# Kernel optimization log

Hardware: AMD Instinct MI355X
Metric: run time of the kernel (lower is better)

## Reference

```python
import jax, jax.numpy as jnp
import numpy as np

B, FEAT, FIELD, K = 16384, 2048, 32, 64

def setup_inputs() -> dict:
    key = jax.random.key(0)
    k1, k2, k3, k4 = jax.random.split(key, 4)
    x = jax.random.normal(k1, (B, FEAT), dtype=jnp.float32)
    # nn.Linear(feature_size, 1): weight [1, FEAT] (use vector), bias [1] (scalar)
    w = jax.random.normal(k2, (FEAT,), dtype=jnp.float32) / np.sqrt(FEAT)
    b = jax.random.normal(k3, (), dtype=jnp.float32)
    # v ~ N(0, 0.01) as in torch.normal(0, 0.01, ...)
    v = 0.01 * jax.random.normal(k4, (FEAT, FIELD, K), dtype=jnp.float32)
    return {"x": x, "w": w, "b": b, "v": v}

def reference(x, w, b, v):
    # linear part: Linear(feature_size, 1).squeeze() -> [B]
    linear_part = x @ w + b  # [B]
    # field_x = tensordot(x, v, dims=1) -> [B, FIELD, K]
    field_x = jnp.einsum('bf,fsk->bsk', x, v)
    # sum_{i<j} sum_k f_i * f_j  ==  0.5 * (||sum_i f_i||^2 - sum_i ||f_i||^2)
    s = field_x.sum(axis=1)                      # [B, K]
    sq = (field_x * field_x).sum(axis=(1, 2))    # [B]
    interaction = 0.5 * ((s * s).sum(axis=-1) - sq)  # [B]
    return jax.nn.sigmoid(linear_part + interaction)
```

## Files before the change

kernel.cpp:

```cpp
#include <hip/hip_runtime.h>
#include <cstdint>
#include <cstddef>

#define B_ROWS 16384
#define FEAT   2048
#define FIELD  32
#define KDIM   64
#define NCOLS  2048
#define NAUG   2176

using half8   = __attribute__((ext_vector_type(8))) _Float16;
using half4   = __attribute__((ext_vector_type(4))) _Float16;
using floatx4 = __attribute__((ext_vector_type(4))) float;

__device__ __forceinline__ void load_lds16(const void* g, void* l) {
  __builtin_amdgcn_global_load_lds((const __attribute__((address_space(1))) void*)g,
                                   (__attribute__((address_space(3))) void*)l, 16, 0, 0);
}

__global__ __launch_bounds__(256) void k_prep(const float* __restrict__ x,
                                              const float* __restrict__ v,
                                              const float* __restrict__ w,
                                              _Float16* __restrict__ xh,
                                              _Float16* __restrict__ vt,
                                              float* __restrict__ arg) {
  const int bb = blockIdx.x;
  const int t = threadIdx.x;
  if (bb < 8192) {
    size_t i = ((size_t)bb * 256 + t) * 16;
    float4 v0 = *(const float4*)(x + i);
    float4 v1 = *(const float4*)(x + i + 4);
    float4 v2 = *(const float4*)(x + i + 8);
    float4 v3 = *(const float4*)(x + i + 12);
    half8 h0 = { (_Float16)v0.x, (_Float16)v0.y, (_Float16)v0.z, (_Float16)v0.w,
                 (_Float16)v1.x, (_Float16)v1.y, (_Float16)v1.z, (_Float16)v1.w };
    half8 h1 = { (_Float16)v2.x, (_Float16)v2.y, (_Float16)v2.z, (_Float16)v2.w,
                 (_Float16)v3.x, (_Float16)v3.y, (_Float16)v3.z, (_Float16)v3.w };
    *(half8*)(xh + i) = h0;
    *(half8*)(xh + i + 8) = h1;
  } else if (bb < 9216) {
    __shared__ _Float16 tile[64 * 68];
    const int b2 = bb - 8192;
    const int f0 = (b2 >> 5) * 64;
    const int n0 = (b2 & 31) * 64;
#pragma unroll
    for (int j = 0; j < 4; ++j) {
      int c = j * 256 + t;
      int row = c >> 4;
      int col = (c & 15) * 4;
      float4 val = *(const float4*)(v + (size_t)(f0 + row) * NCOLS + n0 + col);
      tile[row * 68 + col + 0] = (_Float16)val.x;
      tile[row * 68 + col + 1] = (_Float16)val.y;
      tile[row * 68 + col + 2] = (_Float16)val.z;
      tile[row * 68 + col + 3] = (_Float16)val.w;
    }
    __syncthreads();
#pragma unroll
    for (int j = 0; j < 4; ++j) {
      int c = j * 256 + t;
      int nl = c >> 4;
      int fl = (c & 15) * 4;
      half4 h = { tile[(fl + 0) * 68 + nl], tile[(fl + 1) * 68 + nl],
                  tile[(fl + 2) * 68 + nl], tile[(fl + 3) * 68 + nl] };
      *(half4*)(vt + (size_t)(n0 + nl) * FEAT + f0 + fl) = h;
    }
  } else if (bb < 9728) {
    const int k = t & 63;
    const int f = (bb - 9216) * 4 + (t >> 6);
    float s = 0.f;
#pragma unroll
    for (int si = 0; si < FIELD; ++si) s += v[(size_t)f * NCOLS + si * KDIM + k];
    vt[(size_t)(NCOLS + k) * FEAT + f] = (_Float16)s;
  } else if (bb < 10240) {
    int idx = (bb - 9728) * 256 + t;
    int r = NCOLS + KDIM + (idx >> 11);
    int f = idx & 2047;
    vt[(size_t)r * FEAT + f] = (r == NCOLS + KDIM) ? (_Float16)w[f] : (_Float16)0.f;
  } else {
    arg[(bb - 10240) * 256 + t] = 0.f;
  }
}

__global__ __launch_bounds__(512, 2) void k_gemm(const _Float16* __restrict__ xh,
                                                 const _Float16* __restrict__ vt,
                                                 float* __restrict__ arg) {
  __shared__ __align__(16) _Float16 lds[65536];
  const int tid  = threadIdx.x;
  const int lane = tid & 63;
  const int wave = tid >> 6;
  const int wm   = wave >> 2;
  const int wn   = wave & 3;
  const int lr   = lane & 15;
  const int q    = lane >> 4;

  const int bid = blockIdx.x;
  const int wg  = (bid & 7) * 72 + (bid >> 3);
  const int m0  = (wg & 63) * 256;
  const int n0  = (wg >> 6) * 256;

  int offA[4], offB[4];
#pragma unroll
  for (int f = 0; f < 4; ++f) {
    int L = f * 16 + lr;
    int u = wm * 4 + q;
    offA[f] = L * 64 + ((u ^ (L & 7)) * 8);
  }
#pragma unroll
  for (int g = 0; g < 4; ++g) {
    int L = (wn & 1) * 64 + g * 16 + lr;
    int u = (wn >> 1) * 4 + q;
    offB[g] = L * 64 + ((u ^ (L & 7)) * 8);
  }

  const int L0   = tid >> 3;
  const int u0   = (tid & 7) ^ (L0 & 7);
  const int row0 = (u0 >> 2) * 128 + L0;
  const int kc0  = u0 & 3;
  const _Float16* pA0 = xh + (size_t)(m0 + row0) * FEAT + kc0 * 8;
  const _Float16* pA1 = pA0 + (size_t)64 * FEAT;
  const int rb0 = (n0 + row0      < NAUG) ? n0 + row0      : NAUG - 1;
  const int rb1 = (n0 + row0 + 64 < NAUG) ? n0 + row0 + 64 : NAUG - 1;
  const _Float16* pB0 = vt + (size_t)rb0 * FEAT + kc0 * 8;
  const _Float16* pB1 = vt + (size_t)rb1 * FEAT + kc0 * 8;

  auto stageA = [&](int koff, int seg) {
    load_lds16(pA0 + koff, lds + seg + tid * 8);
    load_lds16(pA1 + koff, lds + seg + 4096 + tid * 8);
  };
  auto stageB = [&](int koff, int seg) {
    load_lds16(pB0 + koff, lds + seg + tid * 8);
    load_lds16(pB1 + koff, lds + seg + 4096 + tid * 8);
  };

  floatx4 acc[8][4] = {};
  half8 af[4], bf[4];

  stageA(0, 0);       stageB(0, 32768);
  stageA(32, 8192);   stageB(32, 40960);
  stageA(64, 16384);  stageB(64, 49152);
  asm volatile("s_waitcnt vmcnt(4)" ::: "memory");
  __builtin_amdgcn_s_barrier();

#define PHASE_TAIL()                                        \
    __builtin_amdgcn_s_barrier();                           \
    asm volatile("s_waitcnt lgkmcnt(0)" ::: "memory");      \
    __builtin_amdgcn_sched_barrier(0);                      \
    __builtin_amdgcn_s_setprio(1)

#define PHASE_END()                                         \
    __builtin_amdgcn_s_setprio(0);                          \
    __builtin_amdgcn_s_barrier()

#pragma unroll 2
  for (int t = 0; t < 32; ++t) {
    const int sA0  = ((t & 1) << 1) * 8192;
    const int sB0  = 32768 + sA0;
    const int sPA1 = ((((t + 1) & 1) << 1) | 1) * 8192;

#pragma unroll
    for (int g = 0; g < 4; ++g) bf[g] = *(const half8*)(lds + sB0 + offB[g]);
#pragma unroll
    for (int f = 0; f < 4; ++f) af[f] = *(const half8*)(lds + sA0 + offA[f]);
    if (t < 31) stageA((t + 1) * 64 + 32, sPA1);
    PHASE_TAIL();
#pragma unroll
    for (int f = 0; f < 4; ++f)
#pragma unroll
      for (int g = 0; g < 4; ++g)
        acc[f][g] = __builtin_amdgcn_mfma_f32_16x16x32_f16(af[f], bf[g],
                                                           acc[f][g], 0, 0, 0);
    PHASE_END();

#pragma unroll
    for (int f = 0; f < 4; ++f) af[f] = *(const half8*)(lds + sA0 + 4096 + offA[f]);
    if (t < 31) stageB((t + 1) * 64 + 32, 32768 + sPA1);
    PHASE_TAIL();
#pragma unroll
    for (int f = 0; f < 4; ++f)
#pragma unroll
      for (int g = 0; g < 4; ++g)
        acc[4 + f][g] = __builtin_amdgcn_mfma_f32_16x16x32_f16(af[f], bf[g],
                                                               acc[4 + f][g], 0, 0, 0);
    PHASE_END();

#pragma unroll
    for (int g = 0; g < 4; ++g) bf[g] = *(const half8*)(lds + sB0 + 8192 + offB[g]);
#pragma unroll
    for (int f = 0; f < 4; ++f) af[f] = *(const half8*)(lds + sA0 + 8192 + offA[f]);
    if (t < 30) stageA((t + 2) * 64, sA0);
    PHASE_TAIL();
#pragma unroll
    for (int f = 0; f < 4; ++f)
#pragma unroll
      for (int g = 0; g < 4; ++g)
        acc[f][g] = __builtin_amdgcn_mfma_f32_16x16x32_f16(af[f], bf[g],
                                                           acc[f][g], 0, 0, 0);
    PHASE_END();

#pragma unroll
    for (int f = 0; f < 4; ++f) af[f] = *(const half8*)(lds + sA0 + 12288 + offA[f]);
    if (t < 30) stageB((t + 2) * 64, sB0);
    __builtin_amdgcn_s_barrier();
    asm volatile("s_waitcnt lgkmcnt(0)" ::: "memory");
    __builtin_amdgcn_sched_barrier(0);
    __builtin_amdgcn_s_setprio(1);
#pragma unroll
    for (int f = 0; f < 4; ++f)
#pragma unroll
      for (int g = 0; g < 4; ++g)
        acc[4 + f][g] = __builtin_amdgcn_mfma_f32_16x16x32_f16(af[f], bf[g],
                                                               acc[4 + f][g], 0, 0, 0);
    __builtin_amdgcn_s_setprio(0);
    if (t < 30) { asm volatile("s_waitcnt vmcnt(4)" ::: "memory"); }
    else        { asm volatile("s_waitcnt vmcnt(0)" ::: "memory"); }
    __builtin_amdgcn_sched_barrier(0);
    __builtin_amdgcn_s_barrier();
  }
#undef PHASE_TAIL
#undef PHASE_END

  const int cq = lane >> 4;
  const int mrow = m0 + wm * 128;
  const int ncol = n0 + wn * 64;
#pragma unroll
  for (int f = 0; f < 8; ++f) {
#pragma unroll
    for (int r = 0; r < 4; ++r) {
      float contrib = 0.f;
#pragma unroll
      for (int g = 0; g < 4; ++g) {
        int col = ncol + g * 16 + lr;
        float vv = acc[f][g][r];
        float qv = vv * vv;
        if (col < NCOLS)                contrib -= 0.5f * qv;
        else if (col < NCOLS + KDIM)    contrib += 0.5f * qv;
        else if (col == NCOLS + KDIM)   contrib += vv;
      }
      contrib += __shfl_xor(contrib, 1);
      contrib += __shfl_xor(contrib, 2);
      contrib += __shfl_xor(contrib, 4);
      contrib += __shfl_xor(contrib, 8);
      if (lr == 0) atomicAdd(&arg[mrow + f * 16 + cq * 4 + r], contrib);
    }
  }
}

__global__ __launch_bounds__(256) void k_fin(const float* __restrict__ arg,
                                             const float* __restrict__ b,
                                             float* __restrict__ out) {
  int i = blockIdx.x * 256 + threadIdx.x;
  float z = arg[i] + b[0];
  out[i] = 1.f / (1.f + __expf(-z));
}

extern "C" void kernel_launch(void* const* d_in, const int* in_sizes, int n_in,
                              void* d_out, int out_size, void* d_ws, size_t ws_size,
                              hipStream_t stream) {
  const float* x = (const float*)d_in[0];
  const float* w = (const float*)d_in[1];
  const float* b = (const float*)d_in[2];
  const float* v = (const float*)d_in[3];
  float* out = (float*)d_out;

  char* ws = (char*)d_ws;
  _Float16* xh  = (_Float16*)ws;
  _Float16* vt  = (_Float16*)(ws + 67108864);
  float*    arg = (float*)(ws + 67108864 + 8912896);

  k_prep<<<10304, 256, 0, stream>>>(x, v, w, xh, vt, arg);
  k_gemm<<<576, 512, 0, stream>>>(xh, vt, arg);
  k_fin<<<64, 256, 0, stream>>>(arg, b, out);
}
```

Baseline: 394.4 us.

## Prefetch LDS fragments one phase ahead in GEMM main loop and split prep kernel

Restructures the GEMM main loop so the A/B register fragments for the next MFMA phase load from LDS during the current phase, using two register sets (afP/afQ, bf0/bf1). Each phase now has one barrier instead of two, and the vmcnt waits are retuned. The aim is to hide LDS read latency behind MFMAs and cut barrier stalls, at the cost of more VGPRs. The prep kernel is also split into separate x-conversion and v-transpose launches, which adds one launch.

Measured after the change: 650.0 us. 64.8% more time.

```diff
diff --git a/kernel.cpp b/kernel.cpp
--- a/kernel.cpp
+++ b/kernel.cpp
@@ -18,31 +18,33 @@
                                    (__attribute__((address_space(3))) void*)l, 16, 0, 0);
 }
 
-__global__ __launch_bounds__(256) void k_prep(const float* __restrict__ x,
-                                              const float* __restrict__ v,
-                                              const float* __restrict__ w,
-                                              _Float16* __restrict__ xh,
-                                              _Float16* __restrict__ vt,
-                                              float* __restrict__ arg) {
+__global__ __launch_bounds__(256) void k_prep_x(const float* __restrict__ x,
+                                                _Float16* __restrict__ xh) {
   const int bb = blockIdx.x;
   const int t = threadIdx.x;
-  if (bb < 8192) {
-    size_t i = ((size_t)bb * 256 + t) * 16;
-    float4 v0 = *(const float4*)(x + i);
-    float4 v1 = *(const float4*)(x + i + 4);
-    float4 v2 = *(const float4*)(x + i + 8);
-    float4 v3 = *(const float4*)(x + i + 12);
-    half8 h0 = { (_Float16)v0.x, (_Float16)v0.y, (_Float16)v0.z, (_Float16)v0.w,
-                 (_Float16)v1.x, (_Float16)v1.y, (_Float16)v1.z, (_Float16)v1.w };
-    half8 h1 = { (_Float16)v2.x, (_Float16)v2.y, (_Float16)v2.z, (_Float16)v2.w,
-                 (_Float16)v3.x, (_Float16)v3.y, (_Float16)v3.z, (_Float16)v3.w };
-    *(half8*)(xh + i) = h0;
-    *(half8*)(xh + i + 8) = h1;
-  } else if (bb < 9216) {
+  size_t i = ((size_t)bb * 256 + t) * 16;
+  float4 v0 = *(const float4*)(x + i);
+  float4 v1 = *(const float4*)(x + i + 4);
+  float4 v2 = *(const float4*)(x + i + 8);
+  float4 v3 = *(const float4*)(x + i + 12);
+  half8 h0 = { (_Float16)v0.x, (_Float16)v0.y, (_Float16)v0.z, (_Float16)v0.w,
+               (_Float16)v1.x, (_Float16)v1.y, (_Float16)v1.z, (_Float16)v1.w };
+  half8 h1 = { (_Float16)v2.x, (_Float16)v2.y, (_Float16)v2.z, (_Float16)v2.w,
+               (_Float16)v3.x, (_Float16)v3.y, (_Float16)v3.z, (_Float16)v3.w };
+  *(half8*)(xh + i) = h0;
+  *(half8*)(xh + i + 8) = h1;
+}
+
+__global__ __launch_bounds__(256) void k_prep_v(const float* __restrict__ v,
+                                                const float* __restrict__ w,
+                                                _Float16* __restrict__ vt,
+                                                float* __restrict__ arg) {
+  const int bb = blockIdx.x;
+  const int t = threadIdx.x;
+  if (bb < 1024) {
     __shared__ _Float16 tile[64 * 68];
-    const int b2 = bb - 8192;
-    const int f0 = (b2 >> 5) * 64;
-    const int n0 = (b2 & 31) * 64;
+    const int f0 = (bb >> 5) * 64;
+    const int n0 = (bb & 31) * 64;
 #pragma unroll
     for (int j = 0; j < 4; ++j) {
       int c = j * 256 + t;
@@ -64,22 +66,30 @@
                   tile[(fl + 2) * 68 + nl], tile[(fl + 3) * 68 + nl] };
       *(half4*)(vt + (size_t)(n0 + nl) * FEAT + f0 + fl) = h;
     }
-  } else if (bb < 9728) {
+  } else if (bb < 1536) {
     const int k = t & 63;
-    const int f = (bb - 9216) * 4 + (t >> 6);
+    const int f = (bb - 1024) * 4 + (t >> 6);
     float s = 0.f;
 #pragma unroll
     for (int si = 0; si < FIELD; ++si) s += v[(size_t)f * NCOLS + si * KDIM + k];
     vt[(size_t)(NCOLS + k) * FEAT + f] = (_Float16)s;
-  } else if (bb < 10240) {
-    int idx = (bb - 9728) * 256 + t;
+  } else if (bb < 2048) {
+    int idx = (bb - 1536) * 256 + t;
     int r = NCOLS + KDIM + (idx >> 11);
     int f = idx & 2047;
     vt[(size_t)r * FEAT + f] = (r == NCOLS + KDIM) ? (_Float16)w[f] : (_Float16)0.f;
   } else {
-    arg[(bb - 10240) * 256 + t] = 0.f;
-  }
-}
+    arg[(bb - 2048) * 256 + t] = 0.f;
+  }
+}
+
+#define NT 32
+
+#define VMCNT(N) asm volatile("s_waitcnt vmcnt(" #N ")" ::: "memory")
+#define LGKM0()  asm volatile("s_waitcnt lgkmcnt(0)" ::: "memory")
+#define SCHED0() __builtin_amdgcn_sched_barrier(0)
+#define BARRIER() __builtin_amdgcn_s_barrier()
+#define PRIO(N) __builtin_amdgcn_s_setprio(N)
 
 __global__ __launch_bounds__(512, 2) void k_gemm(const _Float16* __restrict__ xh,
                                                  const _Float16* __restrict__ vt,
@@ -133,91 +143,93 @@
   };
 
   floatx4 acc[8][4] = {};
-  half8 af[4], bf[4];
+  half8 afP[4], afQ[4], bf0[4], bf1[4];
 
   stageA(0, 0);       stageB(0, 32768);
   stageA(32, 8192);   stageB(32, 40960);
   stageA(64, 16384);  stageB(64, 49152);
-  asm volatile("s_waitcnt vmcnt(4)" ::: "memory");
-  __builtin_amdgcn_s_barrier();
-
-#define PHASE_TAIL()                                        \
-    __builtin_amdgcn_s_barrier();                           \
-    asm volatile("s_waitcnt lgkmcnt(0)" ::: "memory");      \
-    __builtin_amdgcn_sched_barrier(0);                      \
-    __builtin_amdgcn_s_setprio(1)
-
-#define PHASE_END()                                         \
-    __builtin_amdgcn_s_setprio(0);                          \
-    __builtin_amdgcn_s_barrier()
+  VMCNT(8);
+  BARRIER();
+  SCHED0();
+#pragma unroll
+  for (int f = 0; f < 4; ++f) afP[f] = *(const half8*)(lds + offA[f]);
+#pragma unroll
+  for (int g = 0; g < 4; ++g) bf0[g] = *(const half8*)(lds + 32768 + offB[g]);
 
 #pragma unroll 2
-  for (int t = 0; t < 32; ++t) {
-    const int sA0  = ((t & 1) << 1) * 8192;
+  for (int t = 0; t < NT; ++t) {
+    const int sA0  = (t & 1) << 14;
+    const int sA1  = sA0 + 8192;
     const int sB0  = 32768 + sA0;
-    const int sPA1 = ((((t + 1) & 1) << 1) | 1) * 8192;
-
-#pragma unroll
-    for (int g = 0; g < 4; ++g) bf[g] = *(const half8*)(lds + sB0 + offB[g]);
-#pragma unroll
-    for (int f = 0; f < 4; ++f) af[f] = *(const half8*)(lds + sA0 + offA[f]);
-    if (t < 31) stageA((t + 1) * 64 + 32, sPA1);
-    PHASE_TAIL();
-#pragma unroll
-    for (int f = 0; f < 4; ++f)
-#pragma unroll
-      for (int g = 0; g < 4; ++g)
-        acc[f][g] = __builtin_amdgcn_mfma_f32_16x16x32_f16(af[f], bf[g],
+    const int sB1  = sB0 + 8192;
+    const int nsA0 = sA0 ^ 16384;
+    const int nsA1 = nsA0 + 8192;
+    const int nsB0 = 32768 + nsA0;
+    const int nsB1 = nsB0 + 8192;
+
+    BARRIER(); SCHED0();
+#pragma unroll
+    for (int f = 0; f < 4; ++f) afQ[f] = *(const half8*)(lds + sA0 + 4096 + offA[f]);
+    if (t + 1 < NT) stageA((t + 1) * 64 + 32, nsA1);
+    SCHED0(); PRIO(1);
+#pragma unroll
+    for (int f = 0; f < 4; ++f)
+#pragma unroll
+      for (int g = 0; g < 4; ++g)
+        acc[f][g] = __builtin_amdgcn_mfma_f32_16x16x32_f16(afP[f], bf0[g],
                                                            acc[f][g], 0, 0, 0);
-    PHASE_END();
-
-#pragma unroll
-    for (int f = 0; f < 4; ++f) af[f] = *(const half8*)(lds + sA0 + 4096 + offA[f]);
-    if (t < 31) stageB((t + 1) * 64 + 32, 32768 + sPA1);
-    PHASE_TAIL();
-#pragma unroll
-    for (int f = 0; f < 4; ++f)
-#pragma unroll
-      for (int g = 0; g < 4; ++g)
-        acc[4 + f][g] = __builtin_amdgcn_mfma_f32_16x16x32_f16(af[f], bf[g],
+    PRIO(0); SCHED0();
+    LGKM0();
+    if (t < NT - 1) { VMCNT(6); } else { VMCNT(0); }
+
+    BARRIER(); SCHED0();
+#pragma unroll
+    for (int f = 0; f < 4; ++f) afP[f] = *(const half8*)(lds + sA1 + offA[f]);
+#pragma unroll
+    for (int g = 0; g < 4; ++g) bf1[g] = *(const half8*)(lds + sB1 + offB[g]);
+    if (t + 1 < NT) stageB((t + 1) * 64 + 32, nsB1);
+    SCHED0(); PRIO(1);
+#pragma unroll
+    for (int f = 0; f < 4; ++f)
+#pragma unroll
+      for (int g = 0; g < 4; ++g)
+        acc[4 + f][g] = __builtin_amdgcn_mfma_f32_16x16x32_f16(afQ[f], bf0[g],
                                                                acc[4 + f][g], 0, 0, 0);
-    PHASE_END();
-
-#pragma unroll
-    for (int g = 0; g < 4; ++g) bf[g] = *(const half8*)(lds + sB0 + 8192 + offB[g]);
-#pragma unroll
-    for (int f = 0; f < 4; ++f) af[f] = *(const half8*)(lds + sA0 + 8192 + offA[f]);
-    if (t < 30) stageA((t + 2) * 64, sA0);
-    PHASE_TAIL();
-#pragma unroll
-    for (int f = 0; f < 4; ++f)
-#pragma unroll
-      for (int g = 0; g < 4; ++g)
-        acc[f][g] = __builtin_amdgcn_mfma_f32_16x16x32_f16(af[f], bf[g],
+    PRIO(0); SCHED0();
+
+    BARRIER(); SCHED0();
+#pragma unroll
+    for (int f = 0; f < 4; ++f) afQ[f] = *(const half8*)(lds + sA1 + 4096 + offA[f]);
+    if (t + 2 < NT) stageA((t + 2) * 64, sA0);
+    SCHED0(); PRIO(1);
+#pragma unroll
+    for (int f = 0; f < 4; ++f)
+#pragma unroll
+      for (int g = 0; g < 4; ++g)
+        acc[f][g] = __builtin_amdgcn_mfma_f32_16x16x32_f16(afP[f], bf1[g],
                                                            acc[f][g], 0, 0, 0);
-    PHASE_END();
-
-#pragma unroll
-    for (int f = 0; f < 4; ++f) af[f] = *(const half8*)(lds + sA0 + 12288 + offA[f]);
-    if (t < 30) stageB((t + 2) * 64, sB0);
-    __builtin_amdgcn_s_barrier();
-    asm volatile("s_waitcnt lgkmcnt(0)" ::: "memory");
-    __builtin_amdgcn_sched_barrier(0);
-    __builtin_amdgcn_s_setprio(1);
-#pragma unroll
-    for (int f = 0; f < 4; ++f)
-#pragma unroll
-      for (int g = 0; g < 4; ++g)
-        acc[4 + f][g] = __builtin_amdgcn_mfma_f32_16x16x32_f16(af[f], bf[g],
+    PRIO(0); SCHED0();
+    LGKM0();
+    if (t < NT - 2)       { VMCNT(6); }
+    else if (t == NT - 2) { VMCNT(4); }
+
+    BARRIER(); SCHED0();
+    if (t + 1 < NT) {
+#pragma unroll
+      for (int f = 0; f < 4; ++f) afP[f] = *(const half8*)(lds + nsA0 + offA[f]);
+#pragma unroll
+      for (int g = 0; g < 4; ++g) bf0[g] = *(const half8*)(lds + nsB0 + offB[g]);
+    }
+    if (t + 2 < NT) stageB((t + 2) * 64, sB0);
+    SCHED0(); PRIO(1);
+#pragma unroll
+    for (int f = 0; f < 4; ++f)
+#pragma unroll
+      for (int g = 0; g < 4; ++g)
+        acc[4 + f][g] = __builtin_amdgcn_mfma_f32_16x16x32_f16(afQ[f], bf1[g],
                                                                acc[4 + f][g], 0, 0, 0);
-    __builtin_amdgcn_s_setprio(0);
-    if (t < 30) { asm volatile("s_waitcnt vmcnt(4)" ::: "memory"); }
-    else        { asm volatile("s_waitcnt vmcnt(0)" ::: "memory"); }
-    __builtin_amdgcn_sched_barrier(0);
-    __builtin_amdgcn_s_barrier();
-  }
-#undef PHASE_TAIL
-#undef PHASE_END
+    PRIO(0); SCHED0();
+  }
 
   const int cq = lane >> 4;
   const int mrow = m0 + wm * 128;
@@ -267,7 +279,8 @@
   _Float16* vt  = (_Float16*)(ws + 67108864);
   float*    arg = (float*)(ws + 67108864 + 8912896);
 
-  k_prep<<<10304, 256, 0, stream>>>(x, v, w, xh, vt, arg);
+  k_prep_x<<<8192, 256, 0, stream>>>(x, xh);
+  k_prep_v<<<2112, 256, 0, stream>>>(v, w, vt, arg);
   k_gemm<<<576, 512, 0, stream>>>(xh, vt, arg);
   k_fin<<<64, 256, 0, stream>>>(arg, b, out);
 }
```
